# Kernel optimization log

Hardware: AMD Instinct MI355X
Metric: run time of the kernel (lower is better)

The kernel has to match this reference:

```python
import jax, jax.numpy as jnp
import numpy as np

KH, KW = 3, 3

def _grid_offset(H, W):
    # kernel-tap offsets (i, j), ordered row-major like tf.meshgrid(indexing='ij')
    ii, jj = np.meshgrid(np.arange(KH), np.arange(KW), indexing='ij')
    init = np.stack([ii.ravel(), jj.ravel()], axis=-1).astype(np.float32)      # (n, 2)
    pad_h, pad_w = (KH - 1) // 2, (KW - 1) // 2
    gy, gx = np.meshgrid(np.arange(-pad_h, H - pad_h), np.arange(-pad_w, W - pad_w), indexing='ij')
    grid = np.stack([gy, gx], axis=-1).astype(np.float32)                      # (H, W, 2)
    return jnp.asarray(grid[:, :, None, :] + init[None, None, :, :])           # (H, W, n, 2)

def setup_inputs() -> dict:
    key = jax.random.key(0)
    k1, k2, k3 = jax.random.split(key, 3)
    B, H, W_, C, F = 8, 128, 128, 64, 64
    n = KH * KW
    x = jax.random.normal(k1, (B, H, W_, C), dtype=jnp.float32)
    offsets = jax.random.normal(k2, (B, H, W_, 2 * n), dtype=jnp.float32)
    W = jax.random.normal(k3, (n, C, F), dtype=jnp.float32) * 0.02
    b = jnp.zeros((F,), dtype=jnp.float32)
    return {"x": x, "offsets": offsets, "W": W, "b": b}

def reference(x, offsets, W, b):
    B, H, Wd, C = x.shape
    n = KH * KW
    # coords: sampling locations (B, H, W, n, 2), clipped to valid range
    coords = _grid_offset(H, Wd)[None] + offsets.reshape(B, H, Wd, n, 2)
    cy = jnp.clip(coords[..., 0], 0.0, H - 1)
    cx = jnp.clip(coords[..., 1], 0.0, Wd - 1)
    y0 = jnp.floor(cy).astype(jnp.int32)
    y1 = jnp.ceil(cy).astype(jnp.int32)
    x0 = jnp.floor(cx).astype(jnp.int32)
    x1 = jnp.ceil(cx).astype(jnp.int32)
    fy = (cy - y0)[..., None]  # frac along h (matches coords_offset_lt[...,0])
    fx = (cx - x0)[..., None]  # frac along w
    bidx = jnp.arange(B)[:, None, None, None]
    # 4-corner gathers -> (B, H, W, n, C)
    v_lt = x[bidx, y0, x0]
    v_rb = x[bidx, y1, x1]
    v_lb = x[bidx, y0, x1]
    v_rt = x[bidx, y1, x0]
    v_t = v_lt + (v_rt - v_lt) * fy
    v_b = v_lb + (v_rb - v_lb) * fy
    sampled = v_t + (v_b - v_t) * fx                 # (B, H, W, n, C)
    # conv3d with kernel [1,1,n,C,F] VALID == contraction over (n, c)
    out = jnp.einsum('bhwnc,ncf->bhwf', sampled, W) + b
    return out
```

## Files before the change

kernel.cpp:

```cpp
#include <hip/hip_runtime.h>

typedef float v4f __attribute__((ext_vector_type(4)));
typedef float v2f __attribute__((ext_vector_type(2)));
typedef unsigned int uint;
typedef unsigned short ushort;
typedef __attribute__((ext_vector_type(4))) uint u32x4;
typedef __attribute__((ext_vector_type(8))) ushort u16x8;
typedef __attribute__((ext_vector_type(8))) _Float16 h8;
typedef __attribute__((ext_vector_type(16))) float f32x16;

#define NB 8
#define NH 128
#define NW 128
#define NC 64
#define NF 64
#define NTAP 9

__device__ __forceinline__ ushort f2h(float f) {
    return __builtin_bit_cast(ushort, (_Float16)f);
}
__device__ __forceinline__ void g2lds16(const void* g, void* l) {
    __builtin_amdgcn_global_load_lds((__attribute__((address_space(1))) void*)(uintptr_t)g,
                                     (__attribute__((address_space(3))) void*)l, 16, 0, 0);
}

__global__ __launch_bounds__(256) void cvt_x_kernel(const float* __restrict__ x,
                                                    ushort* __restrict__ xh) {
    size_t i = (size_t)blockIdx.x * 256 + threadIdx.x;
    const v4f* src = (const v4f*)x + 2 * i;
    v4f a = src[0], b = src[1];
    u16x8 o;
#pragma unroll
    for (int j = 0; j < 4; j++) { o[j] = f2h(a[j]); o[4 + j] = f2h(b[j]); }
    *(u16x8*)(xh + 8 * i) = o;
}

__global__ __launch_bounds__(256) void prep_w_kernel(const float* __restrict__ wt,
                                                     ushort* __restrict__ wimg) {
    int idx = blockIdx.x * 256 + threadIdx.x;
    int c = idx & 63, f = (idx >> 6) & 63, k = idx >> 12;
    int pg = (c >> 3) ^ (f & 7);
    wimg[(k * 64 + f) * 64 + pg * 8 + (c & 7)] = f2h(wt[(k * 64 + c) * 64 + f]);
}

__global__ __launch_bounds__(256)
void dconv2d_mfma_h(const ushort* __restrict__ xh,
                    const float* __restrict__ offs,
                    const ushort* __restrict__ wimg,
                    const float* __restrict__ bias,
                    float* __restrict__ out)
{
    __shared__ ushort sA[2][128 * 64];
    __shared__ ushort sW[2][64 * 64];

    const int t    = threadIdx.x;
    const int id   = blockIdx.x;
    const int bb   = id & 7;
    const int tile = id >> 3;
    const int h0   = (tile >> 3) * 8;
    const int w0   = (tile & 7) * 16;

    const int p1 = t >> 1;
    const int ch = (t & 1) << 5;
    const int h  = h0 + (p1 >> 4);
    const int w  = w0 + (p1 & 15);

    const int lane = t & 63, wv = t >> 6;
    const int arow = wv * 32 + (lane & 31);
    const int kh   = lane >> 5;

    const float* offp = offs + ((size_t)(bb * NH + h) * NW + w) * (2 * NTAP);
    float offv[18];
#pragma unroll
    for (int j = 0; j < 9; j++) {
        v2f q = *(const v2f*)(offp + 2 * j);
        offv[2 * j] = q[0]; offv[2 * j + 1] = q[1];
    }

    auto stageW = [&](int k, int buf) {
        const char* gb = (const char*)wimg + (size_t)k * 8192;
        char* lb = (char*)(&sW[buf][0]);
#pragma unroll
        for (int it = 0; it < 2; it++)
            g2lds16(gb + it * 4096 + t * 16, lb + it * 4096 + wv * 1024);
    };

    auto issue = [&](int k, u16x8* g00, u16x8* g10, u16x8* g01, u16x8* g11,
                     float& fy, float& fx) {
        const int ky = k / 3, kx = k - 3 * ky;
        float cy = (float)(h - 1 + ky) + offv[2 * k];
        float cx = (float)(w - 1 + kx) + offv[2 * k + 1];
        cy = fminf(fmaxf(cy, 0.f), 127.f);
        cx = fminf(fmaxf(cx, 0.f), 127.f);
        float fy0 = floorf(cy), fx0 = floorf(cx);
        int y0 = (int)fy0,       x0 = (int)fx0;
        int y1 = (int)ceilf(cy), x1 = (int)ceilf(cx);
        fy = cy - fy0; fx = cx - fx0;
        int i00 = ((bb * NH + y0) * NW + x0) * NC + ch;
        int i10 = ((bb * NH + y1) * NW + x0) * NC + ch;
        int i01 = ((bb * NH + y0) * NW + x1) * NC + ch;
        int i11 = ((bb * NH + y1) * NW + x1) * NC + ch;
#pragma unroll
        for (int i = 0; i < 4; i++) {
            g00[i] = *(const u16x8*)(xh + i00 + 8 * i);
            g10[i] = *(const u16x8*)(xh + i10 + 8 * i);
            g01[i] = *(const u16x8*)(xh + i01 + 8 * i);
            g11[i] = *(const u16x8*)(xh + i11 + 8 * i);
        }
    };

    auto commit = [&](int buf, u16x8* g00, u16x8* g10, u16x8* g01, u16x8* g11,
                      float fy, float fx) {
        _Float16 fyh = (_Float16)fy, fxh = (_Float16)fx;
        h8 fy8 = {fyh, fyh, fyh, fyh, fyh, fyh, fyh, fyh};
        h8 fx8 = {fxh, fxh, fxh, fxh, fxh, fxh, fxh, fxh};
#pragma unroll
        for (int i = 0; i < 4; i++) {
            h8 v00 = __builtin_bit_cast(h8, g00[i]);
            h8 v10 = __builtin_bit_cast(h8, g10[i]);
            h8 v01 = __builtin_bit_cast(h8, g01[i]);
            h8 v11 = __builtin_bit_cast(h8, g11[i]);
            h8 vt = v00 + (v10 - v00) * fy8;
            h8 vb = v01 + (v11 - v01) * fy8;
            h8 sv = vt + (vb - vt) * fx8;
            int pg = (((ch >> 3) + i) ^ (p1 & 7));
            *(u16x8*)(&sA[buf][p1 * 64 + pg * 8]) = __builtin_bit_cast(u16x8, sv);
        }
    };

    f32x16 acc0 = (f32x16)0.0f, acc1 = (f32x16)0.0f;

    auto mm = [&](int buf) {
#pragma unroll
        for (int ks = 0; ks < 4; ks++) {
            int g = ks * 2 + kh;
            u32x4 a  = *(const u32x4*)&sA[buf][arow * 64 + ((g ^ (arow & 7)) << 3)];
            u32x4 b0 = *(const u32x4*)&sW[buf][(lane & 31) * 64 + ((g ^ (lane & 7)) << 3)];
            u32x4 b1 = *(const u32x4*)&sW[buf][(32 + (lane & 31)) * 64 + ((g ^ (lane & 7)) << 3)];
            h8 af = __builtin_bit_cast(h8, a);
            acc0 = __builtin_amdgcn_mfma_f32_32x32x16_f16(af, __builtin_bit_cast(h8, b0), acc0, 0, 0, 0);
            acc1 = __builtin_amdgcn_mfma_f32_32x32x16_f16(af, __builtin_bit_cast(h8, b1), acc1, 0, 0, 0);
        }
    };

    stageW(0, 0);
    {
        u16x8 g00[4], g10[4], g01[4], g11[4]; float fy, fx;
        issue(0, g00, g10, g01, g11, fy, fx);
        commit(0, g00, g10, g01, g11, fy, fx);
    }
    __syncthreads();

#pragma unroll
    for (int k = 0; k < NTAP; k++) {
        const int cur = k & 1, nxt = cur ^ 1;
        u16x8 g00[4], g10[4], g01[4], g11[4]; float fy, fx;
        if (k < 8) {
            stageW(k + 1, nxt);
            issue(k + 1, g00, g10, g01, g11, fy, fx);
        }
        mm(cur);
        if (k < 8) {
            commit(nxt, g00, g10, g01, g11, fy, fx);
            __syncthreads();
        }
    }

    const int fcol = lane & 31;
    const float bv0 = bias[fcol], bv1 = bias[32 + fcol];
#pragma unroll
    for (int cb = 0; cb < 2; cb++) {
        f32x16 ac = cb ? acc1 : acc0;
        float bv = cb ? bv1 : bv0;
#pragma unroll
        for (int r = 0; r < 16; r++) {
            int p  = wv * 32 + (r & 3) + 8 * (r >> 2) + 4 * kh;
            int hh = h0 + (p >> 4), ww = w0 + (p & 15);
            out[((size_t)(bb * NH + hh) * NW + ww) * NF + cb * 32 + fcol] = ac[r] + bv;
        }
    }
}

__global__ __launch_bounds__(256)
void dconv2d_fb(const float* __restrict__ xf,
                const float* __restrict__ offs,
                const float* __restrict__ wsf,
                const float* __restrict__ bias,
                float* __restrict__ out)
{
    __shared__ ushort sA[128 * 64];
    __shared__ ushort sW[64 * 64];
    const int t  = threadIdx.x;
    const int bb = blockIdx.z;
    const int h0 = blockIdx.y * 8;
    const int w0 = blockIdx.x * 16;
    const int p1 = t >> 1, ch = (t & 1) << 5;
    const int h = h0 + (p1 >> 4), w = w0 + (p1 & 15);
    const float* offp = offs + ((size_t)(bb * NH + h) * NW + w) * (2 * NTAP);
    const int lane = t & 63, wv = t >> 6;
    const int arow = wv * 32 + (lane & 31);
    const int kh = lane >> 5;
    f32x16 acc0 = (f32x16)0.0f, acc1 = (f32x16)0.0f;

    for (int k = 0; k < NTAP; k++) {
        const float* wp = wsf + (size_t)k * 4096;
#pragma unroll
        for (int it = 0; it < 4; it++) {
            int c = it * 16 + (t >> 4);
            int f4 = (t & 15) * 4;
            v4f v = *(const v4f*)(wp + c * 64 + f4);
#pragma unroll
            for (int j = 0; j < 4; j++) {
                int f = f4 + j;
                sW[f * 64 + (((c >> 3) ^ (f & 7)) << 3) + (c & 7)] = f2h(v[j]);
            }
        }
        const int ky = k / 3, kx = k - 3 * ky;
        float cy = (float)(h - 1 + ky) + offp[2 * k];
        float cx = (float)(w - 1 + kx) + offp[2 * k + 1];
        cy = fminf(fmaxf(cy, 0.f), 127.f);
        cx = fminf(fmaxf(cx, 0.f), 127.f);
        float fy0 = floorf(cy), fx0 = floorf(cx);
        int y0 = (int)fy0, x0 = (int)fx0;
        int y1 = (int)ceilf(cy), x1 = (int)ceilf(cx);
        float fy = cy - fy0, fx = cx - fx0;
        const float* r00 = xf + ((bb * NH + y0) * NW + x0) * NC + ch;
        const float* r10 = xf + ((bb * NH + y1) * NW + x0) * NC + ch;
        const float* r01 = xf + ((bb * NH + y0) * NW + x1) * NC + ch;
        const float* r11 = xf + ((bb * NH + y1) * NW + x1) * NC + ch;
#pragma unroll
        for (int i = 0; i < 8; i++) {
            v4f v00 = *(const v4f*)(r00 + 4 * i);
            v4f v10 = *(const v4f*)(r10 + 4 * i);
            v4f v01 = *(const v4f*)(r01 + 4 * i);
            v4f v11 = *(const v4f*)(r11 + 4 * i);
            v4f vt = v00 + (v10 - v00) * fy;
            v4f vb = v01 + (v11 - v01) * fy;
            v4f sv = vt + (vb - vt) * fx;
            int g = (ch >> 3) + (i >> 1);
            int pg = g ^ (p1 & 7);
#pragma unroll
            for (int e = 0; e < 4; e++)
                sA[p1 * 64 + pg * 8 + (i & 1) * 4 + e] = f2h(sv[e]);
        }
        __syncthreads();
#pragma unroll
        for (int ks = 0; ks < 4; ks++) {
            int g = ks * 2 + kh;
            u32x4 a  = *(const u32x4*)&sA[arow * 64 + ((g ^ (arow & 7)) << 3)];
            u32x4 b0 = *(const u32x4*)&sW[(lane & 31) * 64 + ((g ^ (lane & 7)) << 3)];
            u32x4 b1 = *(const u32x4*)&sW[(32 + (lane & 31)) * 64 + ((g ^ (lane & 7)) << 3)];
            h8 af = __builtin_bit_cast(h8, a);
            acc0 = __builtin_amdgcn_mfma_f32_32x32x16_f16(af, __builtin_bit_cast(h8, b0), acc0, 0, 0, 0);
            acc1 = __builtin_amdgcn_mfma_f32_32x32x16_f16(af, __builtin_bit_cast(h8, b1), acc1, 0, 0, 0);
        }
        __syncthreads();
    }
    const int fcol = lane & 31;
    const float bv0 = bias[fcol], bv1 = bias[32 + fcol];
#pragma unroll
    for (int cb = 0; cb < 2; cb++) {
        f32x16 ac = cb ? acc1 : acc0;
        float bv = cb ? bv1 : bv0;
#pragma unroll
        for (int r = 0; r < 16; r++) {
            int p = wv * 32 + (r & 3) + 8 * (r >> 2) + 4 * kh;
            int hh = h0 + (p >> 4), ww = w0 + (p & 15);
            out[((size_t)(bb * NH + hh) * NW + ww) * NF + cb * 32 + fcol] = ac[r] + bv;
        }
    }
}

extern "C" void kernel_launch(void* const* d_in, const int* in_sizes, int n_in,
                              void* d_out, int out_size, void* d_ws, size_t ws_size,
                              hipStream_t stream) {
    const float* xin  = (const float*)d_in[0];
    const float* offs = (const float*)d_in[1];
    const float* wt   = (const float*)d_in[2];
    const float* bias = (const float*)d_in[3];
    float* out = (float*)d_out;

    const size_t xbytes = (size_t)NB * NH * NW * NC * 2;
    const size_t wbytes = (size_t)NTAP * NC * NF * 2;

    if (ws_size >= xbytes + wbytes) {
        ushort* xh   = (ushort*)d_ws;
        ushort* wimg = (ushort*)((char*)d_ws + xbytes);
        int n8 = NB * NH * NW * NC / 8;
        cvt_x_kernel<<<n8 / 256, 256, 0, stream>>>(xin, xh);
        prep_w_kernel<<<NTAP * NC * NF / 256, 256, 0, stream>>>(wt, wimg);
        dconv2d_mfma_h<<<1024, 256, 0, stream>>>(xh, offs, wimg, bias, out);
    } else {
        dim3 grid(NW / 16, NH / 8, NB);
        dconv2d_fb<<<grid, 256, 0, stream>>>(xin, offs, wt, bias, out);
    }
}
```

Measured before the change: 60.66 us.

## Make each wave own its tile rows, remove block barriers, keep weights in registers

Restructures the main kernel so each wave samples and multiplies only its own 32 pixels. Each wave uses a private double-buffered LDS slice, which removes the block-wide __syncthreads between taps. Weights are prepacked into MFMA operand order and loaded straight into registers, double-buffered per tap, instead of being staged through LDS. The two prep kernels are merged into one launch, and the kernel adds a 2-block occupancy hint and raised priority around the MFMA section. The trade-offs are higher register pressure and the loss of cross-wave sharing of the weight tile, so weights are read from global/L2 once per wave.

```diff
diff --git a/kernel.cpp b/kernel.cpp
--- a/kernel.cpp
+++ b/kernel.cpp
@@ -19,55 +19,59 @@
 __device__ __forceinline__ ushort f2h(float f) {
     return __builtin_bit_cast(ushort, (_Float16)f);
 }
-__device__ __forceinline__ void g2lds16(const void* g, void* l) {
-    __builtin_amdgcn_global_load_lds((__attribute__((address_space(1))) void*)(uintptr_t)g,
-                                     (__attribute__((address_space(3))) void*)l, 16, 0, 0);
-}
-
-__global__ __launch_bounds__(256) void cvt_x_kernel(const float* __restrict__ x,
-                                                    ushort* __restrict__ xh) {
-    size_t i = (size_t)blockIdx.x * 256 + threadIdx.x;
-    const v4f* src = (const v4f*)x + 2 * i;
-    v4f a = src[0], b = src[1];
-    u16x8 o;
-#pragma unroll
-    for (int j = 0; j < 4; j++) { o[j] = f2h(a[j]); o[4 + j] = f2h(b[j]); }
-    *(u16x8*)(xh + 8 * i) = o;
-}
-
-__global__ __launch_bounds__(256) void prep_w_kernel(const float* __restrict__ wt,
-                                                     ushort* __restrict__ wimg) {
-    int idx = blockIdx.x * 256 + threadIdx.x;
-    int c = idx & 63, f = (idx >> 6) & 63, k = idx >> 12;
-    int pg = (c >> 3) ^ (f & 7);
-    wimg[(k * 64 + f) * 64 + pg * 8 + (c & 7)] = f2h(wt[(k * 64 + c) * 64 + f]);
-}
 
 __global__ __launch_bounds__(256)
-void dconv2d_mfma_h(const ushort* __restrict__ xh,
-                    const float* __restrict__ offs,
-                    const ushort* __restrict__ wimg,
-                    const float* __restrict__ bias,
-                    float* __restrict__ out)
+void prep_kernel(const float* __restrict__ x, const float* __restrict__ wt,
+                 ushort* __restrict__ xh, ushort* __restrict__ wr) {
+    int bid = blockIdx.x;
+    if (bid < 4096) {
+        size_t i = (size_t)bid * 256 + threadIdx.x;
+        const v4f* src = (const v4f*)x + 2 * i;
+        v4f a = src[0], b = src[1];
+        u16x8 o;
+#pragma unroll
+        for (int j = 0; j < 4; j++) { o[j] = f2h(a[j]); o[4 + j] = f2h(b[j]); }
+        *(u16x8*)(xh + 8 * i) = o;
+    } else {
+        int idx = (bid - 4096) * 256 + threadIdx.x;
+        int e  = idx & 7;
+        int ln = (idx >> 3) & 63;
+        int fh = (idx >> 9) & 1;
+        int ks = (idx >> 10) & 3;
+        int k  = idx >> 12;
+        int c  = ks * 16 + (ln >> 5) * 8 + e;
+        int f  = fh * 32 + (ln & 31);
+        wr[idx] = f2h(wt[(k * 64 + c) * 64 + f]);
+    }
+}
+
+__global__ __launch_bounds__(256, 2)
+void dconv2d_nb(const ushort* __restrict__ xh,
+                const float* __restrict__ offs,
+                const ushort* __restrict__ wr,
+                const float* __restrict__ bias,
+                float* __restrict__ out)
 {
-    __shared__ ushort sA[2][128 * 64];
-    __shared__ ushort sW[2][64 * 64];
+    __shared__ ushort sA[4][2][32 * 64];
 
     const int t    = threadIdx.x;
+    const int lane = t & 63, wv = t >> 6;
     const int id   = blockIdx.x;
     const int bb   = id & 7;
     const int tile = id >> 3;
     const int h0   = (tile >> 3) * 8;
     const int w0   = (tile & 7) * 16;
 
-    const int p1 = t >> 1;
-    const int ch = (t & 1) << 5;
-    const int h  = h0 + (p1 >> 4);
-    const int w  = w0 + (p1 & 15);
-
-    const int lane = t & 63, wv = t >> 6;
-    const int arow = wv * 32 + (lane & 31);
-    const int kh   = lane >> 5;
+    const int lp = lane >> 1;
+    const int ch = (lane & 1) << 5;
+    const int p  = wv * 32 + lp;
+    const int h  = h0 + (p >> 4);
+    const int w  = w0 + (p & 15);
+
+    const int kh = lane >> 5;
+
+    ushort* A0 = &sA[wv][0][0];
+    ushort* A1 = &sA[wv][1][0];
 
     const float* offp = offs + ((size_t)(bb * NH + h) * NW + w) * (2 * NTAP);
     float offv[18];
@@ -77,16 +81,12 @@
         offv[2 * j] = q[0]; offv[2 * j + 1] = q[1];
     }
 
-    auto stageW = [&](int k, int buf) {
-        const char* gb = (const char*)wimg + (size_t)k * 8192;
-        char* lb = (char*)(&sW[buf][0]);
-#pragma unroll
-        for (int it = 0; it < 2; it++)
-            g2lds16(gb + it * 4096 + t * 16, lb + it * 4096 + wv * 1024);
-    };
-
-    auto issue = [&](int k, u16x8* g00, u16x8* g10, u16x8* g01, u16x8* g11,
-                     float& fy, float& fx) {
+    u16x8 G[16];
+    u32x4 WA[8], WB[8];
+    float FY, FX;
+    f32x16 acc0 = (f32x16)0.0f, acc1 = (f32x16)0.0f;
+
+    auto issueG = [&](int k) {
         const int ky = k / 3, kx = k - 3 * ky;
         float cy = (float)(h - 1 + ky) + offv[2 * k];
         float cx = (float)(w - 1 + kx) + offv[2 * k + 1];
@@ -95,76 +95,79 @@
         float fy0 = floorf(cy), fx0 = floorf(cx);
         int y0 = (int)fy0,       x0 = (int)fx0;
         int y1 = (int)ceilf(cy), x1 = (int)ceilf(cx);
-        fy = cy - fy0; fx = cx - fx0;
+        FY = cy - fy0; FX = cx - fx0;
         int i00 = ((bb * NH + y0) * NW + x0) * NC + ch;
         int i10 = ((bb * NH + y1) * NW + x0) * NC + ch;
         int i01 = ((bb * NH + y0) * NW + x1) * NC + ch;
         int i11 = ((bb * NH + y1) * NW + x1) * NC + ch;
 #pragma unroll
         for (int i = 0; i < 4; i++) {
-            g00[i] = *(const u16x8*)(xh + i00 + 8 * i);
-            g10[i] = *(const u16x8*)(xh + i10 + 8 * i);
-            g01[i] = *(const u16x8*)(xh + i01 + 8 * i);
-            g11[i] = *(const u16x8*)(xh + i11 + 8 * i);
-        }
-    };
-
-    auto commit = [&](int buf, u16x8* g00, u16x8* g10, u16x8* g01, u16x8* g11,
-                      float fy, float fx) {
-        _Float16 fyh = (_Float16)fy, fxh = (_Float16)fx;
+            G[i]      = *(const u16x8*)(xh + i00 + 8 * i);
+            G[4 + i]  = *(const u16x8*)(xh + i10 + 8 * i);
+            G[8 + i]  = *(const u16x8*)(xh + i01 + 8 * i);
+            G[12 + i] = *(const u16x8*)(xh + i11 + 8 * i);
+        }
+    };
+
+    auto commit = [&](ushort* buf) {
+        _Float16 fyh = (_Float16)FY, fxh = (_Float16)FX;
         h8 fy8 = {fyh, fyh, fyh, fyh, fyh, fyh, fyh, fyh};
         h8 fx8 = {fxh, fxh, fxh, fxh, fxh, fxh, fxh, fxh};
 #pragma unroll
         for (int i = 0; i < 4; i++) {
-            h8 v00 = __builtin_bit_cast(h8, g00[i]);
-            h8 v10 = __builtin_bit_cast(h8, g10[i]);
-            h8 v01 = __builtin_bit_cast(h8, g01[i]);
-            h8 v11 = __builtin_bit_cast(h8, g11[i]);
+            h8 v00 = __builtin_bit_cast(h8, G[i]);
+            h8 v10 = __builtin_bit_cast(h8, G[4 + i]);
+            h8 v01 = __builtin_bit_cast(h8, G[8 + i]);
+            h8 v11 = __builtin_bit_cast(h8, G[12 + i]);
             h8 vt = v00 + (v10 - v00) * fy8;
             h8 vb = v01 + (v11 - v01) * fy8;
             h8 sv = vt + (vb - vt) * fx8;
-            int pg = (((ch >> 3) + i) ^ (p1 & 7));
-            *(u16x8*)(&sA[buf][p1 * 64 + pg * 8]) = __builtin_bit_cast(u16x8, sv);
-        }
-    };
-
-    f32x16 acc0 = (f32x16)0.0f, acc1 = (f32x16)0.0f;
-
-    auto mm = [&](int buf) {
+            int gl = (lane & 1) * 4 + i;
+            *(u16x8*)(&buf[lp * 64 + ((gl ^ (lp & 7)) << 3)]) =
+                __builtin_bit_cast(u16x8, sv);
+        }
+    };
+
+    auto loadW = [&](int k, u32x4* Wf) {
+#pragma unroll
+        for (int ks = 0; ks < 4; ks++)
+#pragma unroll
+            for (int fh = 0; fh < 2; fh++)
+                Wf[ks * 2 + fh] = *(const u32x4*)(wr +
+                    ((size_t)((k * 4 + ks) * 2 + fh) * 64 + lane) * 8);
+    };
+
+    auto mm = [&](const ushort* buf, const u32x4* Wf) {
+        __builtin_amdgcn_s_setprio(1);
 #pragma unroll
         for (int ks = 0; ks < 4; ks++) {
             int g = ks * 2 + kh;
-            u32x4 a  = *(const u32x4*)&sA[buf][arow * 64 + ((g ^ (arow & 7)) << 3)];
-            u32x4 b0 = *(const u32x4*)&sW[buf][(lane & 31) * 64 + ((g ^ (lane & 7)) << 3)];
-            u32x4 b1 = *(const u32x4*)&sW[buf][(32 + (lane & 31)) * 64 + ((g ^ (lane & 7)) << 3)];
+            u32x4 a = *(const u32x4*)&buf[(lane & 31) * 64 + ((g ^ (lane & 7)) << 3)];
             h8 af = __builtin_bit_cast(h8, a);
-            acc0 = __builtin_amdgcn_mfma_f32_32x32x16_f16(af, __builtin_bit_cast(h8, b0), acc0, 0, 0, 0);
-            acc1 = __builtin_amdgcn_mfma_f32_32x32x16_f16(af, __builtin_bit_cast(h8, b1), acc1, 0, 0, 0);
-        }
-    };
-
-    stageW(0, 0);
-    {
-        u16x8 g00[4], g10[4], g01[4], g11[4]; float fy, fx;
-        issue(0, g00, g10, g01, g11, fy, fx);
-        commit(0, g00, g10, g01, g11, fy, fx);
-    }
-    __syncthreads();
-
-#pragma unroll
-    for (int k = 0; k < NTAP; k++) {
-        const int cur = k & 1, nxt = cur ^ 1;
-        u16x8 g00[4], g10[4], g01[4], g11[4]; float fy, fx;
-        if (k < 8) {
-            stageW(k + 1, nxt);
-            issue(k + 1, g00, g10, g01, g11, fy, fx);
-        }
-        mm(cur);
-        if (k < 8) {
-            commit(nxt, g00, g10, g01, g11, fy, fx);
-            __syncthreads();
-        }
-    }
+            acc0 = __builtin_amdgcn_mfma_f32_32x32x16_f16(af,
+                       __builtin_bit_cast(h8, Wf[ks * 2 + 0]), acc0, 0, 0, 0);
+            acc1 = __builtin_amdgcn_mfma_f32_32x32x16_f16(af,
+                       __builtin_bit_cast(h8, Wf[ks * 2 + 1]), acc1, 0, 0, 0);
+        }
+        __builtin_amdgcn_s_setprio(0);
+    };
+
+    issueG(0); loadW(0, WA);
+    commit(A0);
+    issueG(1); loadW(1, WB);
+
+#pragma unroll
+    for (int k = 0; k < 8; k++) {
+        ushort* cb = (k & 1) ? A1 : A0;
+        ushort* nb = (k & 1) ? A0 : A1;
+        mm(cb, (k & 1) ? WB : WA);
+        commit(nb);
+        if (k < 7) {
+            issueG(k + 2);
+            loadW(k + 2, (k & 1) ? WB : WA);
+        }
+    }
+    mm(A0, WA);
 
     const int fcol = lane & 31;
     const float bv0 = bias[fcol], bv1 = bias[32 + fcol];
@@ -174,8 +177,8 @@
         float bv = cb ? bv1 : bv0;
 #pragma unroll
         for (int r = 0; r < 16; r++) {
-            int p  = wv * 32 + (r & 3) + 8 * (r >> 2) + 4 * kh;
-            int hh = h0 + (p >> 4), ww = w0 + (p & 15);
+            int pp = wv * 32 + (r & 3) + 8 * (r >> 2) + 4 * kh;
+            int hh = h0 + (pp >> 4), ww = w0 + (pp & 15);
             out[((size_t)(bb * NH + hh) * NW + ww) * NF + cb * 32 + fcol] = ac[r] + bv;
         }
     }
@@ -188,8 +191,8 @@
                 const float* __restrict__ bias,
                 float* __restrict__ out)
 {
-    __shared__ ushort sA[128 * 64];
-    __shared__ ushort sW[64 * 64];
+    __shared__ ushort sAf[128 * 64];
+    __shared__ ushort sWf[64 * 64];
     const int t  = threadIdx.x;
     const int bb = blockIdx.z;
     const int h0 = blockIdx.y * 8;
@@ -212,7 +215,7 @@
 #pragma unroll
             for (int j = 0; j < 4; j++) {
                 int f = f4 + j;
-                sW[f * 64 + (((c >> 3) ^ (f & 7)) << 3) + (c & 7)] = f2h(v[j]);
+                sWf[f * 64 + (((c >> 3) ^ (f & 7)) << 3) + (c & 7)] = f2h(v[j]);
             }
         }
         const int ky = k / 3, kx = k - 3 * ky;
@@ -241,15 +244,15 @@
             int pg = g ^ (p1 & 7);
 #pragma unroll
             for (int e = 0; e < 4; e++)
-                sA[p1 * 64 + pg * 8 + (i & 1) * 4 + e] = f2h(sv[e]);
+                sAf[p1 * 64 + pg * 8 + (i & 1) * 4 + e] = f2h(sv[e]);
         }
         __syncthreads();
 #pragma unroll
         for (int ks = 0; ks < 4; ks++) {
             int g = ks * 2 + kh;
-            u32x4 a  = *(const u32x4*)&sA[arow * 64 + ((g ^ (arow & 7)) << 3)];
-            u32x4 b0 = *(const u32x4*)&sW[(lane & 31) * 64 + ((g ^ (lane & 7)) << 3)];
-            u32x4 b1 = *(const u32x4*)&sW[(32 + (lane & 31)) * 64 + ((g ^ (lane & 7)) << 3)];
+            u32x4 a  = *(const u32x4*)&sAf[arow * 64 + ((g ^ (arow & 7)) << 3)];
+            u32x4 b0 = *(const u32x4*)&sWf[(lane & 31) * 64 + ((g ^ (lane & 7)) << 3)];
+            u32x4 b1 = *(const u32x4*)&sWf[(32 + (lane & 31)) * 64 + ((g ^ (lane & 7)) << 3)];
             h8 af = __builtin_bit_cast(h8, a);
             acc0 = __builtin_amdgcn_mfma_f32_32x32x16_f16(af, __builtin_bit_cast(h8, b0), acc0, 0, 0, 0);
             acc1 = __builtin_amdgcn_mfma_f32_32x32x16_f16(af, __builtin_bit_cast(h8, b1), acc1, 0, 0, 0);
@@ -264,8 +267,8 @@
         float bv = cb ? bv1 : bv0;
 #pragma unroll
         for (int r = 0; r < 16; r++) {
-            int p = wv * 32 + (r & 3) + 8 * (r >> 2) + 4 * kh;
-            int hh = h0 + (p >> 4), ww = w0 + (p & 15);
+            int pp = wv * 32 + (r & 3) + 8 * (r >> 2) + 4 * kh;
+            int hh = h0 + (pp >> 4), ww = w0 + (pp & 15);
             out[((size_t)(bb * NH + hh) * NW + ww) * NF + cb * 32 + fcol] = ac[r] + bv;
         }
     }
@@ -281,15 +284,13 @@
     float* out = (float*)d_out;
 
     const size_t xbytes = (size_t)NB * NH * NW * NC * 2;
-    const size_t wbytes = (size_t)NTAP * NC * NF * 2;
+    const size_t wbytes = (size_t)NTAP * 4 * 2 * 64 * 8 * 2;
 
     if (ws_size >= xbytes + wbytes) {
-        ushort* xh   = (ushort*)d_ws;
-        ushort* wimg = (ushort*)((char*)d_ws + xbytes);
-        int n8 = NB * NH * NW * NC / 8;
-        cvt_x_kernel<<<n8 / 256, 256, 0, stream>>>(xin, xh);
-        prep_w_kernel<<<NTAP * NC * NF / 256, 256, 0, stream>>>(wt, wimg);
-        dconv2d_mfma_h<<<1024, 256, 0, stream>>>(xh, offs, wimg, bias, out);
+        ushort* xh = (ushort*)d_ws;
+        ushort* wr = (ushort*)((char*)d_ws + xbytes);
+        prep_kernel<<<4096 + 144, 256, 0, stream>>>(xin, wt, xh, wr);
+        dconv2d_nb<<<1024, 256, 0, stream>>>(xh, offs, wr, bias, out);
     } else {
         dim3 grid(NW / 16, NH / 8, NB);
         dconv2d_fb<<<grid, 256, 0, stream>>>(xin, offs, wt, bias, out);
```

New measurement: 60.41 us. Within noise of the previous version (-0.4%).
